# Kernel tuning notes

Measured on AMD Instinct MI355X. Metric: run time of the kernel, lower is better.

## Reference

```python
import jax, jax.numpy as jnp
import numpy as np

N, F_IN = 50000, 128      # nodes, input channels
H, C = 4, 32              # attention heads, out channels per head (concat -> H*C = 128)
E = 800000                # directed edges (before self loops)
NEG_SLOPE = 0.2
EPS = 1e-5                # GraphNorm eps


def setup_inputs() -> dict:
    key = jax.random.key(0)
    ks = jax.random.split(key, 9)
    s = 1.0 / np.sqrt(F_IN)
    return {
        "x": jax.random.normal(ks[0], (N, F_IN), jnp.float32),
        "edge_index": jax.random.randint(ks[1], (2, E), 0, N, jnp.int32),
        "W_l": jax.random.uniform(ks[2], (F_IN, H * C), jnp.float32, -s, s),  # source proj
        "W_r": jax.random.uniform(ks[3], (F_IN, H * C), jnp.float32, -s, s),  # target proj
        "att": jax.random.uniform(ks[4], (H, C), jnp.float32, -s, s),         # GATv2 attention vector a
        "bias": jnp.zeros((H * C,), jnp.float32),
        "gn_weight": jnp.ones((H * C,), jnp.float32),
        "gn_bias": jnp.zeros((H * C,), jnp.float32),
        "gn_mean_scale": jnp.ones((H * C,), jnp.float32),
    }


def _gatv2_graphnorm(x, edge_index, W_l, W_r, att, bias, gn_weight, gn_bias, gn_mean_scale):
    n = x.shape[0]
    # add self loops (add_self_loops=True)
    ar = jnp.arange(n, dtype=edge_index.dtype)
    src = jnp.concatenate([edge_index[0], ar])  # message source j
    dst = jnp.concatenate([edge_index[1], ar])  # message target i

    x_l = (x @ W_l).reshape(n, H, C)  # source-side features
    x_r = (x @ W_r).reshape(n, H, C)  # target-side features

    # GATv2 score: a . LeakyReLU(W_l x_j + W_r x_i), per edge per head  [E+N, H]
    e = jax.nn.leaky_relu(x_l[src] + x_r[dst], NEG_SLOPE)
    score = jnp.einsum("ehc,hc->eh", e, att)

    # softmax over each destination's incoming edges (segment softmax)
    smax = jax.ops.segment_max(score, dst, num_segments=n)
    ex = jnp.exp(score - smax[dst])
    denom = jax.ops.segment_sum(ex, dst, num_segments=n)
    alpha = ex / denom[dst]  # [E+N, H]

    # aggregate messages: out_i = sum_j alpha_ij * (W_l x_j)
    out = jax.ops.segment_sum(alpha[:, :, None] * x_l[src], dst, num_segments=n)
    out = out.reshape(n, H * C) + bias  # concat heads

    # GraphNorm (single graph): per-feature mean/var over all nodes
    mean = out.mean(axis=0)
    centered = out - gn_mean_scale * mean
    var = (centered * centered).mean(axis=0)
    return gn_weight * centered * jax.lax.rsqrt(var + EPS) + gn_bias


def reference(x, edge_index, W_l, W_r, att, bias, gn_weight, gn_bias, gn_mean_scale):
    return _gatv2_graphnorm(x, edge_index, W_l, W_r, att, bias, gn_weight, gn_bias, gn_mean_scale)
```

## Files before the change

kernel.cpp:

```cpp
#include <hip/hip_runtime.h>
#include <hip/hip_bf16.h>
#include <math.h>

#define N_NODES 50000
#define F_IN 128
#define HC 128
#define N_EDGES 800000
#define E_TOT (N_EDGES + N_NODES)
#define E_HALF (E_TOT / 2)
#define NEG_SLOPE 0.2f
#define GN_EPS 1e-5f
#define DEG_STRIDE 16
#define CAP 64
#define EB ((E_HALF + 255) / 256)
#define GB ((N_NODES + 127) / 128)

typedef __attribute__((ext_vector_type(8))) short short8;
typedef __attribute__((ext_vector_type(4))) float floatx4;

__device__ inline ushort f2bf(float f) {
    unsigned u = __float_as_uint(f);
    u += 0x7FFF + ((u >> 16) & 1);
    return (ushort)(u >> 16);
}

__global__ __launch_bounds__(256) void edge_k(const int* __restrict__ ei,
                                              int* __restrict__ deg16,
                                              ushort* __restrict__ csrp,
                                              const float* __restrict__ Wl,
                                              const float* __restrict__ Wr,
                                              ushort* __restrict__ wtl,
                                              ushort* __restrict__ wtr) {
    int gid = blockIdx.x * 256 + threadIdx.x;
    if (gid < 16384) {
        int k = gid >> 7, n = gid & 127;
        wtl[n * 128 + k] = f2bf(Wl[gid]);
        wtr[n * 128 + k] = f2bf(Wr[gid]);
    }
    if (gid >= E_HALF) return;
    {
        int src = ei[gid], dst = ei[N_EDGES + gid];
        int r = atomicAdd(&deg16[dst * DEG_STRIDE], 1);
        if (r < CAP) csrp[dst * CAP + r] = (ushort)src;
    }
    {
        int e = gid + E_HALF;
        int src, dst;
        if (e < N_EDGES) { src = ei[e]; dst = ei[N_EDGES + e]; }
        else             { src = dst = e - N_EDGES; }
        int r = atomicAdd(&deg16[dst * DEG_STRIDE], 1);
        if (r < CAP) csrp[dst * CAP + r] = (ushort)src;
    }
}

__global__ __launch_bounds__(512) void gemm2_k(const float* __restrict__ x,
                                               const ushort* __restrict__ wtl,
                                               const ushort* __restrict__ wtr,
                                               ushort* __restrict__ xlb,
                                               ushort* __restrict__ xrb) {
    __shared__ ushort Wt[2][128][136];
    const int tid = threadIdx.x;
#pragma unroll
    for (int i = 0; i < 4; ++i) {
        int idx = i * 512 + tid;
        int n = idx >> 4, k8 = (idx & 15) * 8;
        *(int4*)&Wt[0][n][k8] = *(const int4*)(wtl + n * 128 + k8);
        *(int4*)&Wt[1][n][k8] = *(const int4*)(wtr + n * 128 + k8);
    }
    __syncthreads();

    const int w = tid >> 6, lane = tid & 63;
    const int quad = lane >> 4, l16 = lane & 15;
    const int rbase = blockIdx.x * 128 + w * 16;
    const int grow = rbase + l16;
    const float* ap = x + (size_t)(grow < N_NODES ? grow : (N_NODES - 1)) * F_IN + quad * 8;

    floatx4 accL[8], accR[8];
#pragma unroll
    for (int nt = 0; nt < 8; ++nt) {
        accL[nt] = (floatx4){0.f, 0.f, 0.f, 0.f};
        accR[nt] = (floatx4){0.f, 0.f, 0.f, 0.f};
    }

#pragma unroll
    for (int ks = 0; ks < 4; ++ks) {
        float4 a0 = *(const float4*)(ap + ks * 32 + 0);
        float4 a1 = *(const float4*)(ap + ks * 32 + 4);
        short8 af;
        af[0] = (short)f2bf(a0.x); af[1] = (short)f2bf(a0.y);
        af[2] = (short)f2bf(a0.z); af[3] = (short)f2bf(a0.w);
        af[4] = (short)f2bf(a1.x); af[5] = (short)f2bf(a1.y);
        af[6] = (short)f2bf(a1.z); af[7] = (short)f2bf(a1.w);
#pragma unroll
        for (int nt = 0; nt < 8; ++nt) {
            short8 bfl = *(const short8*)&Wt[0][nt * 16 + l16][ks * 32 + quad * 8];
            short8 bfr = *(const short8*)&Wt[1][nt * 16 + l16][ks * 32 + quad * 8];
            accL[nt] = __builtin_amdgcn_mfma_f32_16x16x32_bf16(af, bfl, accL[nt], 0, 0, 0);
            accR[nt] = __builtin_amdgcn_mfma_f32_16x16x32_bf16(af, bfr, accR[nt], 0, 0, 0);
        }
    }
#pragma unroll
    for (int r = 0; r < 4; ++r) {
        int gro = rbase + quad * 4 + r;
        if (gro < N_NODES) {
            ushort* opl = xlb + (size_t)gro * HC + l16;
            ushort* opr = xrb + (size_t)gro * HC + l16;
#pragma unroll
            for (int nt = 0; nt < 8; ++nt) {
                opl[nt * 16] = f2bf(accL[nt][r]);
                opr[nt * 16] = f2bf(accR[nt][r]);
            }
        }
    }
}

__global__ __launch_bounds__(256) void attn_k(const ushort* __restrict__ xlb,
                                              const ushort* __restrict__ xrb,
                                              const int* __restrict__ deg16,
                                              const ushort* __restrict__ csrp,
                                              const float* __restrict__ att,
                                              const float* __restrict__ bias,
                                              float* __restrict__ out) {
    const int wid = threadIdx.x >> 6, lane = threadIdx.x & 63;
    const int dst = blockIdx.x * 4 + wid;
    if (dst >= N_NODES) return;
    const int e = lane >> 4, s = lane & 15;
    float xrv[8], av[8];
    {
        int4 xv = *(const int4*)(xrb + (size_t)dst * HC + s * 8);
        xrv[0] = __uint_as_float(((unsigned)xv.x) << 16);
        xrv[1] = __uint_as_float(((unsigned)xv.x) & 0xffff0000u);
        xrv[2] = __uint_as_float(((unsigned)xv.y) << 16);
        xrv[3] = __uint_as_float(((unsigned)xv.y) & 0xffff0000u);
        xrv[4] = __uint_as_float(((unsigned)xv.z) << 16);
        xrv[5] = __uint_as_float(((unsigned)xv.z) & 0xffff0000u);
        xrv[6] = __uint_as_float(((unsigned)xv.w) << 16);
        xrv[7] = __uint_as_float(((unsigned)xv.w) & 0xffff0000u);
        float4 a0 = *(const float4*)(att + s * 8);
        float4 a1 = *(const float4*)(att + s * 8 + 4);
        av[0] = a0.x; av[1] = a0.y; av[2] = a0.z; av[3] = a0.w;
        av[4] = a1.x; av[5] = a1.y; av[6] = a1.z; av[7] = a1.w;
    }
    float l = 0.f;
    float acc[8] = {0.f, 0.f, 0.f, 0.f, 0.f, 0.f, 0.f, 0.f};
    const int nk = min(deg16[dst * DEG_STRIDE], CAP);
    const int sv = (int)csrp[dst * CAP + lane];

#define EDGE_STEP(rv, valid)                                                   \
    {                                                                          \
        float f0 = __uint_as_float(((unsigned)(rv).x) << 16);                  \
        float f1 = __uint_as_float(((unsigned)(rv).x) & 0xffff0000u);          \
        float f2 = __uint_as_float(((unsigned)(rv).y) << 16);                  \
        float f3 = __uint_as_float(((unsigned)(rv).y) & 0xffff0000u);          \
        float f4 = __uint_as_float(((unsigned)(rv).z) << 16);                  \
        float f5 = __uint_as_float(((unsigned)(rv).z) & 0xffff0000u);          \
        float f6 = __uint_as_float(((unsigned)(rv).w) << 16);                  \
        float f7 = __uint_as_float(((unsigned)(rv).w) & 0xffff0000u);          \
        float t, part;                                                         \
        t = f0 + xrv[0]; t = t > 0.f ? t : NEG_SLOPE * t; part = av[0] * t;    \
        t = f1 + xrv[1]; t = t > 0.f ? t : NEG_SLOPE * t; part += av[1] * t;   \
        t = f2 + xrv[2]; t = t > 0.f ? t : NEG_SLOPE * t; part += av[2] * t;   \
        t = f3 + xrv[3]; t = t > 0.f ? t : NEG_SLOPE * t; part += av[3] * t;   \
        t = f4 + xrv[4]; t = t > 0.f ? t : NEG_SLOPE * t; part += av[4] * t;   \
        t = f5 + xrv[5]; t = t > 0.f ? t : NEG_SLOPE * t; part += av[5] * t;   \
        t = f6 + xrv[6]; t = t > 0.f ? t : NEG_SLOPE * t; part += av[6] * t;   \
        t = f7 + xrv[7]; t = t > 0.f ? t : NEG_SLOPE * t; part += av[7] * t;   \
        part += __shfl_xor(part, 1, 4);                                        \
        part += __shfl_xor(part, 2, 4);                                        \
        float p = (valid) ? __expf(part) : 0.f;                                \
        l += p;                                                                \
        acc[0] += p * f0; acc[1] += p * f1; acc[2] += p * f2; acc[3] += p * f3;\
        acc[4] += p * f4; acc[5] += p * f5; acc[6] += p * f6; acc[7] += p * f7;\
    }

    int j = 0;
    for (; j + 8 <= nk; j += 8) {
        int s0 = __shfl(sv, j + e, 64);
        int s1 = __shfl(sv, j + 4 + e, 64);
        int4 r0 = *(const int4*)(xlb + (size_t)s0 * HC + s * 8);
        int4 r1 = *(const int4*)(xlb + (size_t)s1 * HC + s * 8);
        EDGE_STEP(r0, true);
        EDGE_STEP(r1, true);
    }
    for (; j < nk; j += 4) {
        int idx = j + e;
        bool valid = idx < nk;
        int s0 = __shfl(sv, valid ? idx : 0, 64);
        int4 r0 = *(const int4*)(xlb + (size_t)s0 * HC + s * 8);
        EDGE_STEP(r0, valid);
    }
#undef EDGE_STEP

    l += __shfl_xor(l, 16, 64);
    l += __shfl_xor(l, 32, 64);
#pragma unroll
    for (int c = 0; c < 8; ++c) {
        acc[c] += __shfl_xor(acc[c], 16, 64);
        acc[c] += __shfl_xor(acc[c], 32, 64);
    }
    if (e == 0) {
        float inv = 1.0f / l;
        float4 b0 = *(const float4*)(bias + s * 8);
        float4 b1 = *(const float4*)(bias + s * 8 + 4);
        float4 o0 = make_float4(acc[0] * inv + b0.x, acc[1] * inv + b0.y,
                                acc[2] * inv + b0.z, acc[3] * inv + b0.w);
        float4 o1 = make_float4(acc[4] * inv + b1.x, acc[5] * inv + b1.y,
                                acc[6] * inv + b1.z, acc[7] * inv + b1.w);
        *(float4*)(out + (size_t)dst * HC + s * 8)     = o0;
        *(float4*)(out + (size_t)dst * HC + s * 8 + 4) = o1;
    }
}

__global__ __launch_bounds__(256) void stats_k(const float* __restrict__ out,
                                               float* __restrict__ gsum,
                                               float* __restrict__ gsumsq) {
    int f = threadIdx.x & 127;
    int half = threadIdx.x >> 7;
    float s = 0.f, s2 = 0.f;
    for (int r = blockIdx.x * 2 + half; r < N_NODES; r += gridDim.x * 2) {
        float v = out[(size_t)r * HC + f];
        s += v; s2 += v * v;
    }
    __shared__ float l1[256], l2[256];
    l1[threadIdx.x] = s; l2[threadIdx.x] = s2;
    __syncthreads();
    if (threadIdx.x < 128) {
        s  = l1[threadIdx.x] + l1[threadIdx.x + 128];
        s2 = l2[threadIdx.x] + l2[threadIdx.x + 128];
        atomicAdd(&gsum[f], s);
        atomicAdd(&gsumsq[f], s2);
    }
}

__global__ __launch_bounds__(256) void norm_k(float* __restrict__ out,
                                              const float* __restrict__ gsum,
                                              const float* __restrict__ gsumsq,
                                              const float* __restrict__ gw,
                                              const float* __restrict__ gb,
                                              const float* __restrict__ gms) {
    int f = threadIdx.x & 127;
    int half = threadIdx.x >> 7;
    const float invN = 1.0f / (float)N_NODES;
    float mean = gsum[f] * invN;
    float msq  = gsumsq[f] * invN;
    float g = gms[f];
    float var = msq - 2.f * g * mean * mean + g * g * mean * mean;
    float rstd = rsqrtf(var + GN_EPS);
    float a = gw[f] * rstd;
    float b = gb[f] - a * g * mean;
    for (int r = blockIdx.x * 2 + half; r < N_NODES; r += gridDim.x * 2) {
        size_t o = (size_t)r * HC + f;
        out[o] = a * out[o] + b;
    }
}

extern "C" void kernel_launch(void* const* d_in, const int* in_sizes, int n_in,
                              void* d_out, int out_size, void* d_ws, size_t ws_size,
                              hipStream_t stream) {
    const float* x    = (const float*)d_in[0];
    const int*   ei   = (const int*)d_in[1];
    const float* Wl   = (const float*)d_in[2];
    const float* Wr   = (const float*)d_in[3];
    const float* att  = (const float*)d_in[4];
    const float* bias = (const float*)d_in[5];
    const float* gw   = (const float*)d_in[6];
    const float* gb   = (const float*)d_in[7];
    const float* gms  = (const float*)d_in[8];
    float* out = (float*)d_out;

    ushort* xlb   = (ushort*)d_ws;
    ushort* xrb   = xlb + (size_t)N_NODES * HC;
    float*  gsum   = (float*)(xrb + (size_t)N_NODES * HC);
    float*  gsumsq = gsum + HC;
    int*    deg16  = (int*)(gsumsq + HC);
    size_t  zero_bytes = (size_t)(HC + HC) * 4 + (size_t)N_NODES * DEG_STRIDE * 4;
    ushort* csrp = (ushort*)(deg16 + (size_t)N_NODES * DEG_STRIDE);
    ushort* wtl  = csrp + (size_t)N_NODES * CAP;
    ushort* wtr  = wtl + 16384;

    hipMemsetAsync((void*)gsum, 0, zero_bytes, stream);
    hipLaunchKernelGGL(edge_k, dim3(EB), dim3(256), 0, stream,
                       ei, deg16, csrp, Wl, Wr, wtl, wtr);
    hipLaunchKernelGGL(gemm2_k, dim3(GB), dim3(512), 0, stream,
                       x, wtl, wtr, xlb, xrb);
    hipLaunchKernelGGL(attn_k, dim3(N_NODES / 4), dim3(256), 0, stream,
                       xlb, xrb, deg16, csrp, att, bias, out);
    hipLaunchKernelGGL(stats_k, dim3(256), dim3(256), 0, stream,
                       out, gsum, gsumsq);
    hipLaunchKernelGGL(norm_k, dim3(512), dim3(256), 0, stream,
                       out, gsum, gsumsq, gw, gb, gms);
}
```

Before: 236.6 us.

## Fuse edge CSR build into GEMM kernel and unroll attention gather loop

Weight transposition moves to a small separate kernel. The edge-bucketing work is folded into the projection GEMM launch as extra blocks, so the atomic CSR build and the MFMA GEMM run concurrently in one grid. The GEMM now uses 256-thread blocks of 64 rows, stages weights through a half-size LDS buffer in two K phases to raise occupancy, and preloads the A fragments up front. The attention gather loop gains a 16-edge unrolled path to put more loads in flight, at the cost of extra registers and an additional kernel launch.

```diff
diff --git a/kernel.cpp b/kernel.cpp
--- a/kernel.cpp
+++ b/kernel.cpp
@@ -12,8 +12,8 @@
 #define GN_EPS 1e-5f
 #define DEG_STRIDE 16
 #define CAP 64
-#define EB ((E_HALF + 255) / 256)
-#define GB ((N_NODES + 127) / 128)
+#define EBF ((E_HALF + 255) / 256)
+#define GB ((N_NODES + 63) / 64)
 
 typedef __attribute__((ext_vector_type(8))) short short8;
 typedef __attribute__((ext_vector_type(4))) float floatx4;
@@ -24,56 +24,62 @@
     return (ushort)(u >> 16);
 }
 
-__global__ __launch_bounds__(256) void edge_k(const int* __restrict__ ei,
-                                              int* __restrict__ deg16,
-                                              ushort* __restrict__ csrp,
-                                              const float* __restrict__ Wl,
-                                              const float* __restrict__ Wr,
-                                              ushort* __restrict__ wtl,
-                                              ushort* __restrict__ wtr) {
-    int gid = blockIdx.x * 256 + threadIdx.x;
-    if (gid < 16384) {
-        int k = gid >> 7, n = gid & 127;
-        wtl[n * 128 + k] = f2bf(Wl[gid]);
-        wtr[n * 128 + k] = f2bf(Wr[gid]);
-    }
-    if (gid >= E_HALF) return;
-    {
-        int src = ei[gid], dst = ei[N_EDGES + gid];
-        int r = atomicAdd(&deg16[dst * DEG_STRIDE], 1);
-        if (r < CAP) csrp[dst * CAP + r] = (ushort)src;
-    }
-    {
-        int e = gid + E_HALF;
-        int src, dst;
-        if (e < N_EDGES) { src = ei[e]; dst = ei[N_EDGES + e]; }
-        else             { src = dst = e - N_EDGES; }
-        int r = atomicAdd(&deg16[dst * DEG_STRIDE], 1);
-        if (r < CAP) csrp[dst * CAP + r] = (ushort)src;
-    }
-}
-
-__global__ __launch_bounds__(512) void gemm2_k(const float* __restrict__ x,
+__global__ __launch_bounds__(256) void wprep_k(const float* __restrict__ Wl,
+                                               const float* __restrict__ Wr,
+                                               ushort* __restrict__ wtl,
+                                               ushort* __restrict__ wtr) {
+    int i = blockIdx.x * 256 + threadIdx.x;
+    int k = i >> 7, n = i & 127;
+    wtl[n * 128 + k] = f2bf(Wl[i]);
+    wtr[n * 128 + k] = f2bf(Wr[i]);
+}
+
+__global__ __launch_bounds__(256, 4) void fg_k(const float* __restrict__ x,
                                                const ushort* __restrict__ wtl,
                                                const ushort* __restrict__ wtr,
                                                ushort* __restrict__ xlb,
-                                               ushort* __restrict__ xrb) {
-    __shared__ ushort Wt[2][128][136];
+                                               ushort* __restrict__ xrb,
+                                               const int* __restrict__ ei,
+                                               int* __restrict__ deg16,
+                                               ushort* __restrict__ csrp) {
+    __shared__ ushort Wt[2][128][68];
     const int tid = threadIdx.x;
-#pragma unroll
-    for (int i = 0; i < 4; ++i) {
-        int idx = i * 512 + tid;
-        int n = idx >> 4, k8 = (idx & 15) * 8;
-        *(int4*)&Wt[0][n][k8] = *(const int4*)(wtl + n * 128 + k8);
-        *(int4*)&Wt[1][n][k8] = *(const int4*)(wtr + n * 128 + k8);
-    }
-    __syncthreads();
+
+    if (blockIdx.x >= GB) {
+        int gid = (blockIdx.x - GB) * 256 + tid;
+        if (gid >= E_HALF) return;
+        {
+            int src = ei[gid], dst = ei[N_EDGES + gid];
+            int r = atomicAdd(&deg16[dst * DEG_STRIDE], 1);
+            if (r < CAP) csrp[dst * CAP + r] = (ushort)src;
+        }
+        {
+            int e = gid + E_HALF;
+            int src, dst;
+            if (e < N_EDGES) { src = ei[e]; dst = ei[N_EDGES + e]; }
+            else             { src = dst = e - N_EDGES; }
+            int r = atomicAdd(&deg16[dst * DEG_STRIDE], 1);
+            if (r < CAP) csrp[dst * CAP + r] = (ushort)src;
+        }
+        return;
+    }
 
     const int w = tid >> 6, lane = tid & 63;
     const int quad = lane >> 4, l16 = lane & 15;
-    const int rbase = blockIdx.x * 128 + w * 16;
+    const int rbase = blockIdx.x * 64 + w * 16;
     const int grow = rbase + l16;
     const float* ap = x + (size_t)(grow < N_NODES ? grow : (N_NODES - 1)) * F_IN + quad * 8;
+
+    short8 af[4];
+#pragma unroll
+    for (int ksg = 0; ksg < 4; ++ksg) {
+        float4 a0 = *(const float4*)(ap + ksg * 32 + 0);
+        float4 a1 = *(const float4*)(ap + ksg * 32 + 4);
+        af[ksg][0] = (short)f2bf(a0.x); af[ksg][1] = (short)f2bf(a0.y);
+        af[ksg][2] = (short)f2bf(a0.z); af[ksg][3] = (short)f2bf(a0.w);
+        af[ksg][4] = (short)f2bf(a1.x); af[ksg][5] = (short)f2bf(a1.y);
+        af[ksg][6] = (short)f2bf(a1.z); af[ksg][7] = (short)f2bf(a1.w);
+    }
 
     floatx4 accL[8], accR[8];
 #pragma unroll
@@ -83,20 +89,28 @@
     }
 
 #pragma unroll
-    for (int ks = 0; ks < 4; ++ks) {
-        float4 a0 = *(const float4*)(ap + ks * 32 + 0);
-        float4 a1 = *(const float4*)(ap + ks * 32 + 4);
-        short8 af;
-        af[0] = (short)f2bf(a0.x); af[1] = (short)f2bf(a0.y);
-        af[2] = (short)f2bf(a0.z); af[3] = (short)f2bf(a0.w);
-        af[4] = (short)f2bf(a1.x); af[5] = (short)f2bf(a1.y);
-        af[6] = (short)f2bf(a1.z); af[7] = (short)f2bf(a1.w);
-#pragma unroll
-        for (int nt = 0; nt < 8; ++nt) {
-            short8 bfl = *(const short8*)&Wt[0][nt * 16 + l16][ks * 32 + quad * 8];
-            short8 bfr = *(const short8*)&Wt[1][nt * 16 + l16][ks * 32 + quad * 8];
-            accL[nt] = __builtin_amdgcn_mfma_f32_16x16x32_bf16(af, bfl, accL[nt], 0, 0, 0);
-            accR[nt] = __builtin_amdgcn_mfma_f32_16x16x32_bf16(af, bfr, accR[nt], 0, 0, 0);
+    for (int s = 0; s < 2; ++s) {
+        if (s) __syncthreads();
+#pragma unroll
+        for (int i = 0; i < 8; ++i) {
+            int idx = i * 256 + tid;
+            int m = idx >> 10;
+            int n = (idx >> 3) & 127;
+            int k8 = (idx & 7) * 8;
+            const ushort* wg = m ? wtr : wtl;
+            *(int4*)&Wt[m][n][k8] = *(const int4*)(wg + n * 128 + s * 64 + k8);
+        }
+        __syncthreads();
+#pragma unroll
+        for (int kp = 0; kp < 2; ++kp) {
+            int ksg = s * 2 + kp;
+#pragma unroll
+            for (int nt = 0; nt < 8; ++nt) {
+                short8 bfl = *(const short8*)&Wt[0][nt * 16 + l16][kp * 32 + quad * 8];
+                short8 bfr = *(const short8*)&Wt[1][nt * 16 + l16][kp * 32 + quad * 8];
+                accL[nt] = __builtin_amdgcn_mfma_f32_16x16x32_bf16(af[ksg], bfl, accL[nt], 0, 0, 0);
+                accR[nt] = __builtin_amdgcn_mfma_f32_16x16x32_bf16(af[ksg], bfr, accR[nt], 0, 0, 0);
+            }
         }
     }
 #pragma unroll
@@ -174,6 +188,20 @@
     }
 
     int j = 0;
+    for (; j + 16 <= nk; j += 16) {
+        int s0 = __shfl(sv, j + e, 64);
+        int s1 = __shfl(sv, j + 4 + e, 64);
+        int s2 = __shfl(sv, j + 8 + e, 64);
+        int s3 = __shfl(sv, j + 12 + e, 64);
+        int4 r0 = *(const int4*)(xlb + (size_t)s0 * HC + s * 8);
+        int4 r1 = *(const int4*)(xlb + (size_t)s1 * HC + s * 8);
+        int4 r2 = *(const int4*)(xlb + (size_t)s2 * HC + s * 8);
+        int4 r3 = *(const int4*)(xlb + (size_t)s3 * HC + s * 8);
+        EDGE_STEP(r0, true);
+        EDGE_STEP(r1, true);
+        EDGE_STEP(r2, true);
+        EDGE_STEP(r3, true);
+    }
     for (; j + 8 <= nk; j += 8) {
         int s0 = __shfl(sv, j + e, 64);
         int s1 = __shfl(sv, j + 4 + e, 64);
@@ -279,10 +307,10 @@
     ushort* wtr  = wtl + 16384;
 
     hipMemsetAsync((void*)gsum, 0, zero_bytes, stream);
-    hipLaunchKernelGGL(edge_k, dim3(EB), dim3(256), 0, stream,
-                       ei, deg16, csrp, Wl, Wr, wtl, wtr);
-    hipLaunchKernelGGL(gemm2_k, dim3(GB), dim3(512), 0, stream,
-                       x, wtl, wtr, xlb, xrb);
+    hipLaunchKernelGGL(wprep_k, dim3(64), dim3(256), 0, stream,
+                       Wl, Wr, wtl, wtr);
+    hipLaunchKernelGGL(fg_k, dim3(GB + EBF), dim3(256), 0, stream,
+                       x, wtl, wtr, xlb, xrb, ei, deg16, csrp);
     hipLaunchKernelGGL(attn_k, dim3(N_NODES / 4), dim3(256), 0, stream,
                        xlb, xrb, deg16, csrp, att, bias, out);
     hipLaunchKernelGGL(stats_k, dim3(256), dim3(256), 0, stream,
```

Result: slower. 243.3 us (+2.9%).

## Partition degree counters and edge buckets by block to reduce atomic contention

Applied to the files above, without the earlier changes.

Edge bucketing now uses 8 partitions selected by block index, each with its own per-node counter and 32-slot bucket, replacing the single padded counter per node. The attention kernel gathers each node's neighbors by prefix-summing the 8 partition counts per lane. The goal is to spread same-address atomic contention across partitions. The gather loop is also unrolled to 16 edges per iteration for more memory-level parallelism. The cost is 8 extra counter reads per node and a larger bucket buffer. Neighbors are still truncated at 64 total.

```diff
diff --git a/kernel.cpp b/kernel.cpp
--- a/kernel.cpp
+++ b/kernel.cpp
@@ -10,8 +10,8 @@
 #define E_HALF (E_TOT / 2)
 #define NEG_SLOPE 0.2f
 #define GN_EPS 1e-5f
-#define DEG_STRIDE 16
-#define CAP 64
+#define NPART 8
+#define CAP8 32
 #define EB ((E_HALF + 255) / 256)
 #define GB ((N_NODES + 127) / 128)
 
@@ -25,8 +25,8 @@
 }
 
 __global__ __launch_bounds__(256) void edge_k(const int* __restrict__ ei,
-                                              int* __restrict__ deg16,
-                                              ushort* __restrict__ csrp,
+                                              int* __restrict__ deg8,
+                                              ushort* __restrict__ csr8,
                                               const float* __restrict__ Wl,
                                               const float* __restrict__ Wr,
                                               ushort* __restrict__ wtl,
@@ -38,18 +38,21 @@
         wtr[n * 128 + k] = f2bf(Wr[gid]);
     }
     if (gid >= E_HALF) return;
+    const int part = blockIdx.x & (NPART - 1);
     {
         int src = ei[gid], dst = ei[N_EDGES + gid];
-        int r = atomicAdd(&deg16[dst * DEG_STRIDE], 1);
-        if (r < CAP) csrp[dst * CAP + r] = (ushort)src;
+        int cell = part * N_NODES + dst;
+        int r = atomicAdd(&deg8[cell], 1);
+        if (r < CAP8) csr8[(size_t)cell * CAP8 + r] = (ushort)src;
     }
     {
         int e = gid + E_HALF;
         int src, dst;
         if (e < N_EDGES) { src = ei[e]; dst = ei[N_EDGES + e]; }
         else             { src = dst = e - N_EDGES; }
-        int r = atomicAdd(&deg16[dst * DEG_STRIDE], 1);
-        if (r < CAP) csrp[dst * CAP + r] = (ushort)src;
+        int cell = part * N_NODES + dst;
+        int r = atomicAdd(&deg8[cell], 1);
+        if (r < CAP8) csr8[(size_t)cell * CAP8 + r] = (ushort)src;
     }
 }
 
@@ -116,8 +119,8 @@
 
 __global__ __launch_bounds__(256) void attn_k(const ushort* __restrict__ xlb,
                                               const ushort* __restrict__ xrb,
-                                              const int* __restrict__ deg16,
-                                              const ushort* __restrict__ csrp,
+                                              const int* __restrict__ deg8,
+                                              const ushort* __restrict__ csr8,
                                               const float* __restrict__ att,
                                               const float* __restrict__ bias,
                                               float* __restrict__ out) {
@@ -141,10 +144,21 @@
         av[0] = a0.x; av[1] = a0.y; av[2] = a0.z; av[3] = a0.w;
         av[4] = a1.x; av[5] = a1.y; av[6] = a1.z; av[7] = a1.w;
     }
+
+    int off = 0, base = 0;
+#pragma unroll
+    for (int p = 0; p < NPART; ++p) {
+        int c = deg8[p * N_NODES + dst];
+        c = min(c, CAP8);
+        if (lane >= base && lane < base + c)
+            off = (p * N_NODES + dst) * CAP8 + (lane - base);
+        base += c;
+    }
+    const int nk = min(base, 64);
+    const int sv = (lane < nk) ? (int)csr8[off] : 0;
+
     float l = 0.f;
     float acc[8] = {0.f, 0.f, 0.f, 0.f, 0.f, 0.f, 0.f, 0.f};
-    const int nk = min(deg16[dst * DEG_STRIDE], CAP);
-    const int sv = (int)csrp[dst * CAP + lane];
 
 #define EDGE_STEP(rv, valid)                                                   \
     {                                                                          \
@@ -174,6 +188,20 @@
     }
 
     int j = 0;
+    for (; j + 16 <= nk; j += 16) {
+        int s0 = __shfl(sv, j + e, 64);
+        int s1 = __shfl(sv, j + 4 + e, 64);
+        int s2 = __shfl(sv, j + 8 + e, 64);
+        int s3 = __shfl(sv, j + 12 + e, 64);
+        int4 r0 = *(const int4*)(xlb + (size_t)s0 * HC + s * 8);
+        int4 r1 = *(const int4*)(xlb + (size_t)s1 * HC + s * 8);
+        int4 r2 = *(const int4*)(xlb + (size_t)s2 * HC + s * 8);
+        int4 r3 = *(const int4*)(xlb + (size_t)s3 * HC + s * 8);
+        EDGE_STEP(r0, true);
+        EDGE_STEP(r1, true);
+        EDGE_STEP(r2, true);
+        EDGE_STEP(r3, true);
+    }
     for (; j + 8 <= nk; j += 8) {
         int s0 = __shfl(sv, j + e, 64);
         int s1 = __shfl(sv, j + 4 + e, 64);
@@ -272,19 +300,19 @@
     ushort* xrb   = xlb + (size_t)N_NODES * HC;
     float*  gsum   = (float*)(xrb + (size_t)N_NODES * HC);
     float*  gsumsq = gsum + HC;
-    int*    deg16  = (int*)(gsumsq + HC);
-    size_t  zero_bytes = (size_t)(HC + HC) * 4 + (size_t)N_NODES * DEG_STRIDE * 4;
-    ushort* csrp = (ushort*)(deg16 + (size_t)N_NODES * DEG_STRIDE);
-    ushort* wtl  = csrp + (size_t)N_NODES * CAP;
+    int*    deg8   = (int*)(gsumsq + HC);
+    size_t  zero_bytes = (size_t)(HC + HC) * 4 + (size_t)NPART * N_NODES * 4;
+    ushort* csr8 = (ushort*)(deg8 + (size_t)NPART * N_NODES);
+    ushort* wtl  = csr8 + (size_t)NPART * N_NODES * CAP8;
     ushort* wtr  = wtl + 16384;
 
     hipMemsetAsync((void*)gsum, 0, zero_bytes, stream);
     hipLaunchKernelGGL(edge_k, dim3(EB), dim3(256), 0, stream,
-                       ei, deg16, csrp, Wl, Wr, wtl, wtr);
+                       ei, deg8, csr8, Wl, Wr, wtl, wtr);
     hipLaunchKernelGGL(gemm2_k, dim3(GB), dim3(512), 0, stream,
                        x, wtl, wtr, xlb, xrb);
     hipLaunchKernelGGL(attn_k, dim3(N_NODES / 4), dim3(256), 0, stream,
-                       xlb, xrb, deg16, csrp, att, bias, out);
+                       xlb, xrb, deg8, csr8, att, bias, out);
     hipLaunchKernelGGL(stats_k, dim3(256), dim3(256), 0, stream,
                        out, gsum, gsumsq);
     hipLaunchKernelGGL(norm_k, dim3(512), dim3(256), 0, stream,
```

Measured after the change: 244.1 us. 3.2% more time.

## Fuse GraphNorm stats and normalize kernels with a grid-wide atomic barrier

Applied to the files above, without the earlier changes.

Merges the statistics reduction and normalization kernels into one persistent kernel of 256 blocks. After each block adds its partial sums atomically, the blocks wait on a global counter barrier and then apply the normalization to the same rows they just read. This removes one kernel launch and may let the second pass hit in cache. The barrier relies on all 256 blocks being co-resident, and a zeroed counter is added to the workspace.

```diff
diff --git a/kernel.cpp b/kernel.cpp
--- a/kernel.cpp
+++ b/kernel.cpp
@@ -14,6 +14,7 @@
 #define CAP 64
 #define EB ((E_HALF + 255) / 256)
 #define GB ((N_NODES + 127) / 128)
+#define SN_B 256
 
 typedef __attribute__((ext_vector_type(8))) short short8;
 typedef __attribute__((ext_vector_type(4))) float floatx4;
@@ -211,44 +212,46 @@
     }
 }
 
-__global__ __launch_bounds__(256) void stats_k(const float* __restrict__ out,
-                                               float* __restrict__ gsum,
-                                               float* __restrict__ gsumsq) {
-    int f = threadIdx.x & 127;
-    int half = threadIdx.x >> 7;
+__global__ __launch_bounds__(256) void statsnorm_k(float* __restrict__ out,
+                                                   float* __restrict__ gsum,
+                                                   float* __restrict__ gsumsq,
+                                                   const float* __restrict__ gw,
+                                                   const float* __restrict__ gb,
+                                                   const float* __restrict__ gms,
+                                                   int* __restrict__ counter) {
+    const int tid = threadIdx.x;
+    const int f = tid & 127, half = tid >> 7;
     float s = 0.f, s2 = 0.f;
-    for (int r = blockIdx.x * 2 + half; r < N_NODES; r += gridDim.x * 2) {
+    for (int r = blockIdx.x * 2 + half; r < N_NODES; r += SN_B * 2) {
         float v = out[(size_t)r * HC + f];
         s += v; s2 += v * v;
     }
     __shared__ float l1[256], l2[256];
-    l1[threadIdx.x] = s; l2[threadIdx.x] = s2;
-    __syncthreads();
-    if (threadIdx.x < 128) {
-        s  = l1[threadIdx.x] + l1[threadIdx.x + 128];
-        s2 = l2[threadIdx.x] + l2[threadIdx.x + 128];
-        atomicAdd(&gsum[f], s);
-        atomicAdd(&gsumsq[f], s2);
-    }
-}
-
-__global__ __launch_bounds__(256) void norm_k(float* __restrict__ out,
-                                              const float* __restrict__ gsum,
-                                              const float* __restrict__ gsumsq,
-                                              const float* __restrict__ gw,
-                                              const float* __restrict__ gb,
-                                              const float* __restrict__ gms) {
-    int f = threadIdx.x & 127;
-    int half = threadIdx.x >> 7;
+    l1[tid] = s; l2[tid] = s2;
+    __syncthreads();
+    if (tid < 128) {
+        atomicAdd(&gsum[f], l1[tid] + l1[tid + 128]);
+        atomicAdd(&gsumsq[f], l2[tid] + l2[tid + 128]);
+    }
+    __syncthreads();
+    if (tid == 0) {
+        __hip_atomic_fetch_add(counter, 1, __ATOMIC_ACQ_REL, __HIP_MEMORY_SCOPE_AGENT);
+        int c;
+        do {
+            c = __hip_atomic_load(counter, __ATOMIC_ACQUIRE, __HIP_MEMORY_SCOPE_AGENT);
+            if (c < SN_B) __builtin_amdgcn_s_sleep(8);
+        } while (c < SN_B);
+    }
+    __syncthreads();
     const float invN = 1.0f / (float)N_NODES;
-    float mean = gsum[f] * invN;
-    float msq  = gsumsq[f] * invN;
+    float mean = __hip_atomic_load(&gsum[f],   __ATOMIC_RELAXED, __HIP_MEMORY_SCOPE_AGENT) * invN;
+    float msq  = __hip_atomic_load(&gsumsq[f], __ATOMIC_RELAXED, __HIP_MEMORY_SCOPE_AGENT) * invN;
     float g = gms[f];
     float var = msq - 2.f * g * mean * mean + g * g * mean * mean;
     float rstd = rsqrtf(var + GN_EPS);
     float a = gw[f] * rstd;
     float b = gb[f] - a * g * mean;
-    for (int r = blockIdx.x * 2 + half; r < N_NODES; r += gridDim.x * 2) {
+    for (int r = blockIdx.x * 2 + half; r < N_NODES; r += SN_B * 2) {
         size_t o = (size_t)r * HC + f;
         out[o] = a * out[o] + b;
     }
@@ -270,10 +273,11 @@
 
     ushort* xlb   = (ushort*)d_ws;
     ushort* xrb   = xlb + (size_t)N_NODES * HC;
-    float*  gsum   = (float*)(xrb + (size_t)N_NODES * HC);
-    float*  gsumsq = gsum + HC;
-    int*    deg16  = (int*)(gsumsq + HC);
-    size_t  zero_bytes = (size_t)(HC + HC) * 4 + (size_t)N_NODES * DEG_STRIDE * 4;
+    float*  gsum    = (float*)(xrb + (size_t)N_NODES * HC);
+    float*  gsumsq  = gsum + HC;
+    int*    counter = (int*)(gsumsq + HC);
+    int*    deg16   = counter + 4;
+    size_t  zero_bytes = (size_t)(HC + HC + 4) * 4 + (size_t)N_NODES * DEG_STRIDE * 4;
     ushort* csrp = (ushort*)(deg16 + (size_t)N_NODES * DEG_STRIDE);
     ushort* wtl  = csrp + (size_t)N_NODES * CAP;
     ushort* wtr  = wtl + 16384;
@@ -285,8 +289,6 @@
                        x, wtl, wtr, xlb, xrb);
     hipLaunchKernelGGL(attn_k, dim3(N_NODES / 4), dim3(256), 0, stream,
                        xlb, xrb, deg16, csrp, att, bias, out);
-    hipLaunchKernelGGL(stats_k, dim3(256), dim3(256), 0, stream,
-                       out, gsum, gsumsq);
-    hipLaunchKernelGGL(norm_k, dim3(512), dim3(256), 0, stream,
-                       out, gsum, gsumsq, gw, gb, gms);
-}
+    hipLaunchKernelGGL(statsnorm_k, dim3(SN_B), dim3(256), 0, stream,
+                       out, gsum, gsumsq, gw, gb, gms, counter);
+}
```

Result: slower. 247.1 us (+4.5%).
